# Optimization experiments

Hardware: AMD Instinct MI355X
Metric: run time of the kernel (lower is better)

The kernel has to match this reference:

```python
import jax, jax.numpy as jnp
import numpy as np

VOCAB = 100000
DIM = 128
B = 16384
C_MAX = 10
K_NEG = 5


def setup_inputs() -> dict:
    key = jax.random.key(0)
    k1, k2, k3, k4, k5, k6 = jax.random.split(key, 6)
    bound = 0.5 / DIM
    return {
        "target_words": jax.random.randint(k1, (B,), 0, VOCAB),
        "context_words": jax.random.randint(k2, (B, C_MAX), 0, VOCAB),
        "context_lens": jax.random.randint(k3, (B,), 0, C_MAX + 1),
        "negative_words": jax.random.randint(k4, (B, K_NEG), 0, VOCAB),
        # input embeddings init: uniform(-0.5/dim, 0.5/dim); output init zeros in the
        # original, but we use small random values so gradients/scores are non-trivial.
        "in_emb": jax.random.uniform(k5, (VOCAB, DIM), jnp.float32, -bound, bound),
        "out_emb": jax.random.normal(k6, (VOCAB, DIM), jnp.float32) * 0.01,
    }


def reference(target_words, context_words, context_lens, negative_words, in_emb, out_emb):
    t = in_emb[target_words]                      # (B, D)
    c = out_emb[context_words]                    # (B, C, D)
    n = out_emb[negative_words]                   # (B, K, D)

    pos_scores = jnp.einsum("bd,bcd->bc", t, c)   # (B, C)
    neg_scores = jnp.einsum("bd,bkd->bk", t, n)   # (B, K)

    mask = (jnp.arange(C_MAX)[None, :] < context_lens[:, None]).astype(t.dtype)
    lens = context_lens.astype(t.dtype)
    has_ctx = lens > 0

    # per-sample mean of -logsigmoid over valid contexts; skip samples with 0 contexts
    pos_per = -jnp.sum(jax.nn.log_sigmoid(pos_scores) * mask, axis=1)
    pos_per = jnp.where(has_ctx, pos_per / jnp.maximum(lens, 1.0), 0.0)

    neg_per = -jnp.mean(jax.nn.log_sigmoid(-neg_scores), axis=1)
    neg_per = jnp.where(has_ctx, neg_per, 0.0)    # original `continue` skips negatives too

    positive_loss = jnp.sum(pos_per) / B
    negative_loss = jnp.sum(neg_per) / B
    return positive_loss, negative_loss
```

## Files before the change

kernel.cpp:

```cpp
#include <hip/hip_runtime.h>
#include <math.h>
#include <stdint.h>

#define VOCAB 100000
#define DIM   128
#define BATCH 16384
#define CMAX  10
#define KNEG  5

typedef float f32x4 __attribute__((ext_vector_type(4)));

__device__ __forceinline__ float log_sigmoid(float x) {
    return fminf(x, 0.0f) - log1pf(expf(-fabsf(x)));
}

#define DPP_ADD_STEP(v, ctrl)                                                  \
    v += __int_as_float(__builtin_amdgcn_update_dpp(                           \
        0, __float_as_int(v), (ctrl), 0xF, 0xF, false))

__device__ __forceinline__ float dpp_reduce32_to_lane31(float v) {
    DPP_ADD_STEP(v, 0x111);
    DPP_ADD_STEP(v, 0x112);
    DPP_ADD_STEP(v, 0x114);
    DPP_ADD_STEP(v, 0x118);
    DPP_ADD_STEP(v, 0x142);
    return v;
}

__global__ __launch_bounds__(256) void score_loss_kernel(
    const int*   __restrict__ tgt,
    const int*   __restrict__ ctx,
    const int*   __restrict__ lens,
    const int*   __restrict__ neg,
    const float* __restrict__ in_emb,
    const float* __restrict__ out_emb,
    float2*      __restrict__ per_sample,
    float*       __restrict__ out)
{
    const int tid  = threadIdx.x;
    const int lane = tid & 63;
    const int sub  = lane & 31;
    const int half = lane >> 5;
    const int b    = (blockIdx.x * 256 + tid) >> 6;
    const int bu   = __builtin_amdgcn_readfirstlane(b);

    if (blockIdx.x == 0 && tid < 2) out[tid] = 0.0f;

    const int len    = lens[bu];
    const int t_word = tgt[bu];
    int ctxw[CMAX];
#pragma unroll
    for (int c = 0; c < CMAX; ++c) ctxw[c] = ctx[bu * CMAX + c];
    int negw[KNEG];
#pragma unroll
    for (int k = 0; k < KNEG; ++k) negw[k] = neg[bu * KNEG + k];

    int words[8];
#pragma unroll
    for (int jj = 0; jj < 8; ++jj) {
        const int w0 = (jj < len) ? ctxw[jj] : negw[0];
        int w1;
        if (jj < 2)       w1 = ((8 + jj) < len) ? ctxw[8 + jj] : negw[0];
        else if (jj < 7)  w1 = negw[jj - 2];
        else              w1 = negw[0];
        words[jj] = half ? w1 : w0;
    }

    asm volatile("s_waitcnt vmcnt(0)" ::: "memory");

    const uint32_t sub16 = (uint32_t)sub * 16u;
    f32x4 tv;
    {
        uint32_t off = (uint32_t)t_word * (DIM * 4u) + sub16;
        asm volatile("global_load_dwordx4 %0, %1, %2"
                     : "=v"(tv) : "v"(off), "s"(in_emb));
    }
    f32x4 rv[8];
#pragma unroll
    for (int jj = 0; jj < 8; ++jj) {
        uint32_t off = (uint32_t)words[jj] * (DIM * 4u) + sub16;
        asm volatile("global_load_dwordx4 %0, %1, %2"
                     : "=v"(rv[jj]) : "v"(off), "s"(out_emb));
    }

    float p[8];
#pragma unroll
    for (int jj = 0; jj < 8; ++jj) {
        asm volatile("s_waitcnt vmcnt(%[cnt])"
                     : "+v"(rv[jj]), "+v"(tv)
                     : [cnt] "i"(7 - jj)
                     : "memory");
        float d = tv.x * rv[jj].x + tv.y * rv[jj].y +
                  tv.z * rv[jj].z + tv.w * rv[jj].w;
        p[jj] = dpp_reduce32_to_lane31(d);
    }

    float bc[8];
#pragma unroll
    for (int jj = 0; jj < 8; ++jj) bc[jj] = __shfl(p[jj], 31, 32);

    const int sel = sub & 7;
    float a0 = (sel & 1) ? bc[1] : bc[0];
    float a1 = (sel & 1) ? bc[3] : bc[2];
    float a2 = (sel & 1) ? bc[5] : bc[4];
    float a3 = (sel & 1) ? bc[7] : bc[6];
    float b0 = (sel & 2) ? a1 : a0;
    float b1 = (sel & 2) ? a3 : a2;
    float s  = (sel & 4) ? b1 : b0;

    const int  j        = half * 8 + sel;
    const bool neg_slot = (j >= CMAX) && (j < CMAX + KNEG);
    const bool active   = (sub < 8);

    float v    = log_sigmoid(neg_slot ? -s : s);
    float posc = (active && j < len)  ? v : 0.0f;
    float negc = (active && neg_slot) ? v : 0.0f;

    posc += __shfl_xor(posc, 1, 64);
    posc += __shfl_xor(posc, 2, 64);
    posc += __shfl_xor(posc, 4, 64);
    posc += __shfl_xor(posc, 32, 64);
    negc += __shfl_xor(negc, 1, 64);
    negc += __shfl_xor(negc, 2, 64);
    negc += __shfl_xor(negc, 4, 64);
    negc += __shfl_xor(negc, 32, 64);

    if (lane == 0) {
        float2 r;
        if (len > 0) {
            r.x = -posc / (float)len;
            r.y = -negc * (1.0f / KNEG);
        } else {
            r.x = 0.0f;
            r.y = 0.0f;
        }
        per_sample[b] = r;
    }
}

__global__ __launch_bounds__(256) void reduce_kernel(
    const float2* __restrict__ per_sample,
    float*        __restrict__ out)
{
    const int tid = threadIdx.x;
    const int b   = blockIdx.x * 256 + tid;

    const float2 pr = per_sample[b];
    float pos = pr.x;
    float neg = pr.y;

#pragma unroll
    for (int m = 32; m >= 1; m >>= 1) {
        pos += __shfl_xor(pos, m, 64);
        neg += __shfl_xor(neg, m, 64);
    }
    __shared__ float s_pos[4];
    __shared__ float s_neg[4];
    const int wave = tid >> 6;
    if ((tid & 63) == 0) { s_pos[wave] = pos; s_neg[wave] = neg; }
    __syncthreads();
    if (tid == 0) {
        float ps = s_pos[0] + s_pos[1] + s_pos[2] + s_pos[3];
        float ns = s_neg[0] + s_neg[1] + s_neg[2] + s_neg[3];
        atomicAdd(&out[0], ps * (1.0f / BATCH));
        atomicAdd(&out[1], ns * (1.0f / BATCH));
    }
}

extern "C" void kernel_launch(void* const* d_in, const int* in_sizes, int n_in,
                              void* d_out, int out_size, void* d_ws, size_t ws_size,
                              hipStream_t stream) {
    const int*   tgt     = (const int*)  d_in[0];
    const int*   ctx     = (const int*)  d_in[1];
    const int*   lens    = (const int*)  d_in[2];
    const int*   neg     = (const int*)  d_in[3];
    const float* in_emb  = (const float*)d_in[4];
    const float* out_emb = (const float*)d_in[5];
    float* out          = (float*)d_out;
    float2* per_sample  = (float2*)d_ws;

    score_loss_kernel<<<BATCH / 4, 256, 0, stream>>>(
        tgt, ctx, lens, neg, in_emb, out_emb, per_sample, out);

    reduce_kernel<<<BATCH / 256, 256, 0, stream>>>(per_sample, out);
}
```

Baseline: 127.2 us.

## Specialize score kernel per context length to skip padded row gathers

Dispatches on the per-sample context length through a templated body, so each wave gathers only the LEN+KNEG rows it actually needs, packed in pairs across the two half-waves, instead of always loading 8 rows per half. Samples with zero contexts now skip all embedding loads. The per-row staggered waitcnt pipelining is replaced by one wait on all loads, and the switch adds ten code paths, which grows code size.

New measurement: 127.2 us. Within noise of the previous version (+0.0%).

```diff
diff --git a/kernel.cpp b/kernel.cpp
--- a/kernel.cpp
+++ b/kernel.cpp
@@ -25,6 +25,85 @@
     DPP_ADD_STEP(v, 0x118);
     DPP_ADD_STEP(v, 0x142);
     return v;
+}
+
+template<int LEN>
+__device__ __forceinline__ void body(
+    int t_word, const int (&ctxw)[CMAX], const int (&negw)[KNEG],
+    const float* __restrict__ in_emb, const float* __restrict__ out_emb,
+    int sub, int half, uint32_t sub16, float2& res)
+{
+    constexpr int ROWS  = LEN + KNEG;
+    constexpr int SLOTS = (ROWS + 1) & ~1;
+    constexpr int NI    = SLOTS / 2;
+
+    int wr[SLOTS];
+#pragma unroll
+    for (int r = 0; r < SLOTS; ++r) {
+        const int ci  = (r < CMAX) ? r : 0;
+        int       ni  = (r >= LEN) ? (r - LEN) : 0;
+        ni = (ni > KNEG - 1) ? (KNEG - 1) : ni;
+        wr[r] = (r < LEN) ? ctxw[ci] : negw[ni];
+    }
+
+    int w[NI];
+#pragma unroll
+    for (int jj = 0; jj < NI; ++jj)
+        w[jj] = half ? wr[2 * jj + 1] : wr[2 * jj];
+
+    f32x4 tv;
+    asm volatile("global_load_dwordx4 %0, %1, %2"
+                 : "=v"(tv)
+                 : "v"((uint32_t)t_word * 512u + sub16), "s"(in_emb));
+    f32x4 rv[NI];
+#pragma unroll
+    for (int jj = 0; jj < NI; ++jj) {
+        asm volatile("global_load_dwordx4 %0, %1, %2"
+                     : "=v"(rv[jj])
+                     : "v"((uint32_t)w[jj] * 512u + sub16), "s"(out_emb));
+    }
+    asm volatile("s_waitcnt vmcnt(0)" ::: "memory");
+    __builtin_amdgcn_sched_barrier(0);
+
+    float bc[8];
+#pragma unroll
+    for (int jj = 0; jj < 8; ++jj) bc[jj] = 0.0f;
+#pragma unroll
+    for (int jj = 0; jj < NI; ++jj) {
+        float d = tv.x * rv[jj].x + tv.y * rv[jj].y +
+                  tv.z * rv[jj].z + tv.w * rv[jj].w;
+        float p = dpp_reduce32_to_lane31(d);
+        bc[jj] = __shfl(p, 31, 32);
+    }
+
+    const int sel = sub & 7;
+    float a0 = (sel & 1) ? bc[1] : bc[0];
+    float a1 = (sel & 1) ? bc[3] : bc[2];
+    float a2 = (sel & 1) ? bc[5] : bc[4];
+    float a3 = (sel & 1) ? bc[7] : bc[6];
+    float b0 = (sel & 2) ? a1 : a0;
+    float b1 = (sel & 2) ? a3 : a2;
+    float sv = (sel & 4) ? b1 : b0;
+
+    const int  r      = 2 * sel + half;
+    const bool is_neg = (r >= LEN);
+    const bool active = (sub < 8) && (r < ROWS);
+
+    float v    = log_sigmoid(is_neg ? -sv : sv);
+    float posc = (active && !is_neg) ? v : 0.0f;
+    float negc = (active &&  is_neg) ? v : 0.0f;
+
+    posc += __shfl_xor(posc, 1, 64);
+    posc += __shfl_xor(posc, 2, 64);
+    posc += __shfl_xor(posc, 4, 64);
+    posc += __shfl_xor(posc, 32, 64);
+    negc += __shfl_xor(negc, 1, 64);
+    negc += __shfl_xor(negc, 2, 64);
+    negc += __shfl_xor(negc, 4, 64);
+    negc += __shfl_xor(negc, 32, 64);
+
+    res.x = -posc * (1.0f / (float)LEN);
+    res.y = -negc * (1.0f / KNEG);
 }
 
 __global__ __launch_bounds__(256) void score_loss_kernel(
@@ -55,87 +134,24 @@
 #pragma unroll
     for (int k = 0; k < KNEG; ++k) negw[k] = neg[bu * KNEG + k];
 
-    int words[8];
-#pragma unroll
-    for (int jj = 0; jj < 8; ++jj) {
-        const int w0 = (jj < len) ? ctxw[jj] : negw[0];
-        int w1;
-        if (jj < 2)       w1 = ((8 + jj) < len) ? ctxw[8 + jj] : negw[0];
-        else if (jj < 7)  w1 = negw[jj - 2];
-        else              w1 = negw[0];
-        words[jj] = half ? w1 : w0;
-    }
-
-    asm volatile("s_waitcnt vmcnt(0)" ::: "memory");
-
     const uint32_t sub16 = (uint32_t)sub * 16u;
-    f32x4 tv;
-    {
-        uint32_t off = (uint32_t)t_word * (DIM * 4u) + sub16;
-        asm volatile("global_load_dwordx4 %0, %1, %2"
-                     : "=v"(tv) : "v"(off), "s"(in_emb));
-    }
-    f32x4 rv[8];
-#pragma unroll
-    for (int jj = 0; jj < 8; ++jj) {
-        uint32_t off = (uint32_t)words[jj] * (DIM * 4u) + sub16;
-        asm volatile("global_load_dwordx4 %0, %1, %2"
-                     : "=v"(rv[jj]) : "v"(off), "s"(out_emb));
-    }
-
-    float p[8];
-#pragma unroll
-    for (int jj = 0; jj < 8; ++jj) {
-        asm volatile("s_waitcnt vmcnt(%[cnt])"
-                     : "+v"(rv[jj]), "+v"(tv)
-                     : [cnt] "i"(7 - jj)
-                     : "memory");
-        float d = tv.x * rv[jj].x + tv.y * rv[jj].y +
-                  tv.z * rv[jj].z + tv.w * rv[jj].w;
-        p[jj] = dpp_reduce32_to_lane31(d);
-    }
-
-    float bc[8];
-#pragma unroll
-    for (int jj = 0; jj < 8; ++jj) bc[jj] = __shfl(p[jj], 31, 32);
-
-    const int sel = sub & 7;
-    float a0 = (sel & 1) ? bc[1] : bc[0];
-    float a1 = (sel & 1) ? bc[3] : bc[2];
-    float a2 = (sel & 1) ? bc[5] : bc[4];
-    float a3 = (sel & 1) ? bc[7] : bc[6];
-    float b0 = (sel & 2) ? a1 : a0;
-    float b1 = (sel & 2) ? a3 : a2;
-    float s  = (sel & 4) ? b1 : b0;
-
-    const int  j        = half * 8 + sel;
-    const bool neg_slot = (j >= CMAX) && (j < CMAX + KNEG);
-    const bool active   = (sub < 8);
-
-    float v    = log_sigmoid(neg_slot ? -s : s);
-    float posc = (active && j < len)  ? v : 0.0f;
-    float negc = (active && neg_slot) ? v : 0.0f;
-
-    posc += __shfl_xor(posc, 1, 64);
-    posc += __shfl_xor(posc, 2, 64);
-    posc += __shfl_xor(posc, 4, 64);
-    posc += __shfl_xor(posc, 32, 64);
-    negc += __shfl_xor(negc, 1, 64);
-    negc += __shfl_xor(negc, 2, 64);
-    negc += __shfl_xor(negc, 4, 64);
-    negc += __shfl_xor(negc, 32, 64);
-
-    if (lane == 0) {
-        float2 r;
-        if (len > 0) {
-            r.x = -posc / (float)len;
-            r.y = -negc * (1.0f / KNEG);
-        } else {
-            r.x = 0.0f;
-            r.y = 0.0f;
-        }
-        per_sample[b] = r;
-    }
+    float2 res; res.x = 0.0f; res.y = 0.0f;
+
+    switch (len) {
+    case 1:  body<1> (t_word, ctxw, negw, in_emb, out_emb, sub, half, sub16, res); break;
+    case 2:  body<2> (t_word, ctxw, negw, in_emb, out_emb, sub, half, sub16, res); break;
+    case 3:  body<3> (t_word, ctxw, negw, in_emb, out_emb, sub, half, sub16, res); break;
+    case 4:  body<4> (t_word, ctxw, negw, in_emb, out_emb, sub, half, sub16, res); break;
+    case 5:  body<5> (t_word, ctxw, negw, in_emb, out_emb, sub, half, sub16, res); break;
+    case 6:  body<6> (t_word, ctxw, negw, in_emb, out_emb, sub, half, sub16, res); break;
+    case 7:  body<7> (t_word, ctxw, negw, in_emb, out_emb, sub, half, sub16, res); break;
+    case 8:  body<8> (t_word, ctxw, negw, in_emb, out_emb, sub, half, sub16, res); break;
+    case 9:  body<9> (t_word, ctxw, negw, in_emb, out_emb, sub, half, sub16, res); break;
+    case 10: body<10>(t_word, ctxw, negw, in_emb, out_emb, sub, half, sub16, res); break;
+    default: break;
+    }
+
+    if (lane == 0) per_sample[b] = res;
 }
 
 __global__ __launch_bounds__(256) void reduce_kernel(
```
